# Kernel tuning notes

Hardware: AMD Instinct MI355X
Metric: run time of the kernel (lower is better)

## Reference

```python
import jax, jax.numpy as jnp
import numpy as np

N_NODES = 20000
N_EDGES = 320000
D_IN = 256      # n_source_nodes (input feature dim)
HEADS = 4
HEAD_DIM = 64   # n_target_nodes // heads
D_OUT = HEADS * HEAD_DIM  # n_target_nodes = 256
EDGE_DIM = 1


def setup_inputs() -> dict:
    key = jax.random.key(0)
    ks = jax.random.split(key, 12)
    s = 0.05
    return {
        "x": jax.random.normal(ks[0], (N_NODES, D_IN), jnp.float32),
        "edge_index": jax.random.randint(ks[1], (2, N_EDGES), 0, N_NODES, jnp.int64),
        "edge_attr": jax.random.normal(ks[2], (N_EDGES, EDGE_DIM), jnp.float32),
        # TransformerConv params (weights stored [in, out]; PyG Linear defaults: q/k/v have bias, edge lin has no bias, skip lin has bias)
        "Wq": jax.random.normal(ks[3], (D_IN, D_OUT), jnp.float32) * s,
        "bq": jnp.zeros((D_OUT,), jnp.float32),
        "Wk": jax.random.normal(ks[4], (D_IN, D_OUT), jnp.float32) * s,
        "bk": jnp.zeros((D_OUT,), jnp.float32),
        "Wv": jax.random.normal(ks[5], (D_IN, D_OUT), jnp.float32) * s,
        "bv": jnp.zeros((D_OUT,), jnp.float32),
        "We": jax.random.normal(ks[6], (EDGE_DIM, D_OUT), jnp.float32) * s,
        "Wskip": jax.random.normal(ks[7], (D_IN, D_OUT), jnp.float32) * s,
        "bskip": jnp.zeros((D_OUT,), jnp.float32),
        # GraphNorm params
        "gn_weight": jnp.ones((D_OUT,), jnp.float32),
        "gn_bias": jnp.zeros((D_OUT,), jnp.float32),
        "gn_mean_scale": jnp.ones((D_OUT,), jnp.float32),
    }


def reference(x, edge_index, edge_attr, Wq, bq, Wk, bk, Wv, bv, We, Wskip, bskip, gn_weight, gn_bias, gn_mean_scale):
    N = x.shape[0]
    src, dst = edge_index[0], edge_index[1]  # message flows src -> dst (source_to_target)

    q = (x @ Wq + bq).reshape(N, HEADS, HEAD_DIM)
    k = (x @ Wk + bk).reshape(N, HEADS, HEAD_DIM)
    v = (x @ Wv + bv).reshape(N, HEADS, HEAD_DIM)
    e = (edge_attr @ We).reshape(-1, HEADS, HEAD_DIM)  # [E, H, C]

    k_j = k[src] + e                                   # [E, H, C]
    alpha = jnp.einsum('ehc,ehc->eh', q[dst], k_j) / jnp.sqrt(jnp.float32(HEAD_DIM))

    # segment softmax over edges sharing the same target node
    a_max = jax.ops.segment_max(alpha, dst, num_segments=N)[dst]
    a_exp = jnp.exp(alpha - a_max)
    a_sum = jax.ops.segment_sum(a_exp, dst, num_segments=N)[dst]
    att = a_exp / (a_sum + 1e-16)                      # [E, H]

    msg = (v[src] + e) * att[..., None]                # [E, H, C]
    out = jax.ops.segment_sum(msg, dst, num_segments=N).reshape(N, D_OUT)
    out = out + x @ Wskip + bskip                      # root/skip connection (beta=False)

    # GraphNorm (single graph): weight*(x - alpha*mean)/sqrt(var+eps) + bias
    mean = out.mean(axis=0)
    centered = out - gn_mean_scale * mean
    var = jnp.mean(centered * centered, axis=0)
    out = gn_weight * centered * jax.lax.rsqrt(var + 1e-5) + gn_bias

    out = jax.nn.relu(out)
    xt = out.T @ out                                   # [D_OUT, D_OUT]
    xt_min, xt_max = jnp.min(xt), jnp.max(xt)
    return (xt - xt_min) / (xt_max - xt_min + 1e-8)
```

## Files before the change

kernel.cpp:

```cpp
#include <hip/hip_runtime.h>
#include <math.h>

#define N_NODES 20000
#define N_EDGES 320000
#define SK 20480

typedef short short8 __attribute__((ext_vector_type(8)));
typedef float f32x4 __attribute__((ext_vector_type(4)));

static __device__ __forceinline__ unsigned short f2bf(float f) {
    unsigned int u = __float_as_uint(f);
    u = (u + 0x7FFF + ((u >> 16) & 1)) >> 16;
    return (unsigned short)u;
}
static __device__ __forceinline__ float b2f(unsigned short u) {
    return __uint_as_float((unsigned int)u << 16);
}

__global__ __launch_bounds__(256) void conv_x_k(const float* __restrict__ x,
                                                unsigned short* __restrict__ xb)
{
    const int t8 = blockIdx.x * 256 + threadIdx.x;
    const size_t base = (size_t)t8 * 8;
    if (base >= (size_t)N_NODES * 256) return;
    const float4 f0 = *(const float4*)(x + base);
    const float4 f1 = *(const float4*)(x + base + 4);
    ushort4 u0, u1;
    u0.x = f2bf(f0.x); u0.y = f2bf(f0.y); u0.z = f2bf(f0.z); u0.w = f2bf(f0.w);
    u1.x = f2bf(f1.x); u1.y = f2bf(f1.y); u1.z = f2bf(f1.z); u1.w = f2bf(f1.w);
    *(ushort4*)(xb + base) = u0;
    *(ushort4*)(xb + base + 4) = u1;
}

__global__ __launch_bounds__(256) void conv_w_k(const float* __restrict__ Wq,
                                                const float* __restrict__ Wk,
                                                const float* __restrict__ Wv,
                                                const float* __restrict__ Wsk,
                                                const float* __restrict__ bq,
                                                const float* __restrict__ bk,
                                                const float* __restrict__ bv,
                                                const float* __restrict__ bsk,
                                                unsigned short* __restrict__ wT,
                                                float* __restrict__ bias_all)
{
    const int b = blockIdx.x;
    const int kk = threadIdx.x;
    const int wi = b >> 8, n = b & 255;
    const float* W = (wi == 0) ? Wq : (wi == 1) ? Wk : (wi == 2) ? Wv : Wsk;
    wT[(size_t)b * 256 + kk] = f2bf(W[(size_t)kk * 256 + n]);
    if (kk == 0) {
        const float* bb = (wi == 0) ? bq : (wi == 1) ? bk : (wi == 2) ? bv : bsk;
        bias_all[b] = bb[n];
    }
}

__global__ __launch_bounds__(512, 2) void gemm_qkvs(const unsigned short* __restrict__ xb,
                                                    const unsigned short* __restrict__ wT,
                                                    const float* __restrict__ bias_all,
                                                    float* __restrict__ qb,
                                                    unsigned short* __restrict__ kb,
                                                    unsigned short* __restrict__ vb,
                                                    float* __restrict__ ob)
{
    __shared__ __align__(16) unsigned short As[(128 + 256) * 80];
    unsigned short* Bs = As + 128 * 80;
    float* stage = (float*)As;

    const int tid  = threadIdx.x;
    const int lane = tid & 63;
    const int w    = tid >> 6;
    const int wm = w >> 2, wn = w & 3;
    const int row0 = blockIdx.x * 128;
    const int wsel = blockIdx.y;
    const int colG = wsel * 256;
    const int ar = tid >> 2, ak = (tid & 3) * 16;
    const int br = tid >> 1, bk = (tid & 1) * 32;
    const int fr = lane & 15, fk = (lane >> 4) * 8, lg = lane >> 4;

    f32x4 acc[4][4] = {};

    for (int k0 = 0; k0 < 256; k0 += 64) {
        int gr = row0 + ar; gr = gr < N_NODES ? gr : N_NODES - 1;
        const unsigned short* ap = xb + (size_t)gr * 256 + k0 + ak;
        const uint4 a0 = *(const uint4*)ap;
        const uint4 a1 = *(const uint4*)(ap + 8);
        const unsigned short* bp = wT + (size_t)(colG + br) * 256 + k0 + bk;
        const uint4 b0 = *(const uint4*)bp;
        const uint4 b1 = *(const uint4*)(bp + 8);
        const uint4 b2 = *(const uint4*)(bp + 16);
        const uint4 b3 = *(const uint4*)(bp + 24);
        __syncthreads();
        *(uint4*)&As[ar * 80 + ak]     = a0;
        *(uint4*)&As[ar * 80 + ak + 8] = a1;
        unsigned short* bsp = &Bs[br * 80 + bk];
        *(uint4*)bsp        = b0;
        *(uint4*)(bsp + 8)  = b1;
        *(uint4*)(bsp + 16) = b2;
        *(uint4*)(bsp + 24) = b3;
        __syncthreads();
#pragma unroll
        for (int ks = 0; ks < 2; ++ks) {
            short8 af[4], bf[4];
#pragma unroll
            for (int m = 0; m < 4; ++m)
                af[m] = *(const short8*)&As[(wm * 64 + m * 16 + fr) * 80 + ks * 32 + fk];
#pragma unroll
            for (int n = 0; n < 4; ++n)
                bf[n] = *(const short8*)&Bs[(wn * 64 + n * 16 + fr) * 80 + ks * 32 + fk];
#pragma unroll
            for (int m = 0; m < 4; ++m)
#pragma unroll
                for (int n = 0; n < 4; ++n)
                    acc[m][n] = __builtin_amdgcn_mfma_f32_16x16x32_bf16(af[m], bf[n], acc[m][n], 0, 0, 0);
        }
    }
    __syncthreads();

    float badd[4];
#pragma unroll
    for (int n = 0; n < 4; ++n) badd[n] = bias_all[colG + wn * 64 + n * 16 + fr];

    float* st = stage + w * 1024;
#pragma unroll
    for (int m = 0; m < 4; ++m) {
#pragma unroll
        for (int n = 0; n < 4; ++n)
#pragma unroll
            for (int r = 0; r < 4; ++r)
                st[(lg * 4 + r) * 64 + n * 16 + fr] = acc[m][n][r] + badd[n];
#pragma unroll
        for (int it = 0; it < 4; ++it) {
            const int lrow = it * 4 + lg;
            const f32x4 c4 = *(const f32x4*)&st[lrow * 64 + fr * 4];
            const int grow = row0 + wm * 64 + m * 16 + lrow;
            if (grow < N_NODES) {
                const size_t idx = (size_t)grow * 256 + wn * 64 + fr * 4;
                if (wsel == 0) {
                    float4 o; o.x = c4[0]; o.y = c4[1]; o.z = c4[2]; o.w = c4[3];
                    *(float4*)(qb + idx) = o;
                } else if (wsel == 3) {
                    float4 o; o.x = c4[0]; o.y = c4[1]; o.z = c4[2]; o.w = c4[3];
                    *(float4*)(ob + idx) = o;
                } else {
                    ushort4 u;
                    u.x = f2bf(c4[0]); u.y = f2bf(c4[1]); u.z = f2bf(c4[2]); u.w = f2bf(c4[3]);
                    if (wsel == 1) *(ushort4*)(kb + idx) = u;
                    else           *(ushort4*)(vb + idx) = u;
                }
            }
        }
    }
}

__global__ void count_deg(const int* __restrict__ dst, int* __restrict__ deg)
{
    const int e = blockIdx.x * 256 + threadIdx.x;
    if (e < N_EDGES) atomicAdd(&deg[dst[e]], 1);
}

__global__ __launch_bounds__(1024) void scan_k(const int* __restrict__ deg,
                                               int* __restrict__ row_start)
{
    const int tid = threadIdx.x;
    const int lane = tid & 63, wid = tid >> 6;
    const int CH = 20;
    const int base = tid * CH;
    int local[CH];
    int s = 0;
#pragma unroll
    for (int i = 0; i < CH; ++i) {
        const int idx = base + i;
        const int d = (idx < N_NODES) ? deg[idx] : 0;
        local[i] = s;
        s += d;
    }
    int v = s;
#pragma unroll
    for (int off = 1; off < 64; off <<= 1) {
        const int t = __shfl_up(v, off);
        if (lane >= off) v += t;
    }
    __shared__ int wsum[16];
    if (lane == 63) wsum[wid] = v;
    __syncthreads();
    if (tid == 0) {
        int r = 0;
        for (int i = 0; i < 16; ++i) { const int t = wsum[i]; wsum[i] = r; r += t; }
    }
    __syncthreads();
    const int excl = v - s + wsum[wid];
#pragma unroll
    for (int i = 0; i < CH; ++i) {
        const int idx = base + i;
        if (idx < N_NODES) row_start[idx] = excl + local[i];
    }
    if (tid == 1023) row_start[N_NODES] = excl + s;
}

__global__ void fill_csr(const int* __restrict__ dst, const int* __restrict__ src,
                         const float* __restrict__ ea,
                         const int* __restrict__ row_start,
                         int* __restrict__ cursor, int2* __restrict__ ekv)
{
    const int e = blockIdx.x * 256 + threadIdx.x;
    if (e < N_EDGES) {
        const int d = dst[e];
        const int p = atomicAdd(&cursor[d], 1);
        int2 pk;
        pk.x = src[e];
        pk.y = __float_as_int(ea[e]);
        ekv[row_start[d] + p] = pk;
    }
}

__global__ __launch_bounds__(256) void attn_k(const float* __restrict__ q,
                                              const unsigned short* __restrict__ kb,
                                              const unsigned short* __restrict__ vb,
                                              const float* __restrict__ We,
                                              const int* __restrict__ row_start,
                                              const int2* __restrict__ ekv,
                                              float* __restrict__ out)
{
    const int wid  = threadIdx.x >> 6;
    const int lane = threadIdx.x & 63;
    const int n = blockIdx.x * 4 + wid;
    if (n >= N_NODES) return;

    const float4 qf  = *(const float4*)(q + (size_t)n * 256 + lane * 4);
    const float4 we4 = *(const float4*)(We + lane * 4);
    const int rs = row_start[n], re = row_start[n + 1];

    float ssum = 0.f;
    float ax = 0.f, ay = 0.f, az = 0.f, aw = 0.f;

    int s = rs;
    for (; s + 2 <= re; s += 2) {
        const int2 p0 = ekv[s];
        const int2 p1 = ekv[s + 1];
        int sn0 = p0.x, sn1 = p1.x;
        sn0 = ((unsigned)sn0 < N_NODES) ? sn0 : 0;
        sn1 = ((unsigned)sn1 < N_NODES) ? sn1 : 0;
        const float a0 = __int_as_float(p0.y), a1 = __int_as_float(p1.y);
        const ushort4 k0 = *(const ushort4*)(kb + (size_t)sn0 * 256 + lane * 4);
        const ushort4 v0 = *(const ushort4*)(vb + (size_t)sn0 * 256 + lane * 4);
        const ushort4 k1 = *(const ushort4*)(kb + (size_t)sn1 * 256 + lane * 4);
        const ushort4 v1 = *(const ushort4*)(vb + (size_t)sn1 * 256 + lane * 4);

        float p = qf.x * (b2f(k0.x) + a0 * we4.x) + qf.y * (b2f(k0.y) + a0 * we4.y)
                + qf.z * (b2f(k0.z) + a0 * we4.z) + qf.w * (b2f(k0.w) + a0 * we4.w);
        p += __shfl_xor(p, 1); p += __shfl_xor(p, 2);
        p += __shfl_xor(p, 4); p += __shfl_xor(p, 8);
        float wgt = __expf(p * 0.125f);
        ssum += wgt;
        ax += wgt * (b2f(v0.x) + a0 * we4.x);
        ay += wgt * (b2f(v0.y) + a0 * we4.y);
        az += wgt * (b2f(v0.z) + a0 * we4.z);
        aw += wgt * (b2f(v0.w) + a0 * we4.w);

        p = qf.x * (b2f(k1.x) + a1 * we4.x) + qf.y * (b2f(k1.y) + a1 * we4.y)
          + qf.z * (b2f(k1.z) + a1 * we4.z) + qf.w * (b2f(k1.w) + a1 * we4.w);
        p += __shfl_xor(p, 1); p += __shfl_xor(p, 2);
        p += __shfl_xor(p, 4); p += __shfl_xor(p, 8);
        wgt = __expf(p * 0.125f);
        ssum += wgt;
        ax += wgt * (b2f(v1.x) + a1 * we4.x);
        ay += wgt * (b2f(v1.y) + a1 * we4.y);
        az += wgt * (b2f(v1.z) + a1 * we4.z);
        aw += wgt * (b2f(v1.w) + a1 * we4.w);
    }
    if (s < re) {
        const int2 p0 = ekv[s];
        int sn0 = p0.x;
        sn0 = ((unsigned)sn0 < N_NODES) ? sn0 : 0;
        const float a0 = __int_as_float(p0.y);
        const ushort4 k0 = *(const ushort4*)(kb + (size_t)sn0 * 256 + lane * 4);
        const ushort4 v0 = *(const ushort4*)(vb + (size_t)sn0 * 256 + lane * 4);
        float p = qf.x * (b2f(k0.x) + a0 * we4.x) + qf.y * (b2f(k0.y) + a0 * we4.y)
                + qf.z * (b2f(k0.z) + a0 * we4.z) + qf.w * (b2f(k0.w) + a0 * we4.w);
        p += __shfl_xor(p, 1); p += __shfl_xor(p, 2);
        p += __shfl_xor(p, 4); p += __shfl_xor(p, 8);
        const float wgt = __expf(p * 0.125f);
        ssum += wgt;
        ax += wgt * (b2f(v0.x) + a0 * we4.x);
        ay += wgt * (b2f(v0.y) + a0 * we4.y);
        az += wgt * (b2f(v0.z) + a0 * we4.z);
        aw += wgt * (b2f(v0.w) + a0 * we4.w);
    }
    const float inv = 1.f / (ssum + 1e-16f);
    const float4 sk = *(const float4*)(out + (size_t)n * 256 + lane * 4);
    float4 o;
    o.x = ax * inv + sk.x;
    o.y = ay * inv + sk.y;
    o.z = az * inv + sk.z;
    o.w = aw * inv + sk.w;
    *(float4*)(out + (size_t)n * 256 + lane * 4) = o;
}

__global__ __launch_bounds__(256) void gn_stats_k(const float* __restrict__ out,
                                                  float* __restrict__ gstats)
{
    const int c = threadIdx.x;
    float s = 0.f, s2 = 0.f;
    for (int r = blockIdx.x; r < N_NODES; r += gridDim.x) {
        const float vv = out[(size_t)r * 256 + c];
        s += vv; s2 += vv * vv;
    }
    atomicAdd(&gstats[c], s);
    atomicAdd(&gstats[256 + c], s2);
}

__global__ __launch_bounds__(256) void norm_relu_T(const float* __restrict__ ob,
                                                   const float* __restrict__ gstats,
                                                   const float* __restrict__ gw,
                                                   const float* __restrict__ gb,
                                                   const float* __restrict__ gms,
                                                   unsigned short* __restrict__ obT)
{
    __shared__ unsigned short tile[256][72];
    __shared__ float smu[256], swi[256], sbd[256];
    const int t = threadIdx.x;
    const int r0 = blockIdx.x * 64;
    {
        const float invN = 1.f / (float)N_NODES;
        const float mean = gstats[t] * invN;
        const float exx  = gstats[256 + t] * invN;
        const float mu   = gms[t] * mean;
        const float var  = exx - 2.f * mu * mean + mu * mu;
        smu[t] = mu;
        swi[t] = gw[t] * rsqrtf(var + 1e-5f);
        sbd[t] = gb[t];
    }
    __syncthreads();
    const int rr = t >> 2;
    const int row = r0 + rr;
#pragma unroll
    for (int it = 0; it < 16; ++it) {
        const int col = it * 16 + (t & 3) * 4;
        float4 f = make_float4(0.f, 0.f, 0.f, 0.f);
        if (row < N_NODES) f = *(const float4*)(ob + (size_t)row * 256 + col);
        ushort4 u;
        if (row < N_NODES) {
            u.x = f2bf(fmaxf((f.x - smu[col + 0]) * swi[col + 0] + sbd[col + 0], 0.f));
            u.y = f2bf(fmaxf((f.y - smu[col + 1]) * swi[col + 1] + sbd[col + 1], 0.f));
            u.z = f2bf(fmaxf((f.z - smu[col + 2]) * swi[col + 2] + sbd[col + 2], 0.f));
            u.w = f2bf(fmaxf((f.w - smu[col + 3]) * swi[col + 3] + sbd[col + 3], 0.f));
        } else { u.x = u.y = u.z = u.w = 0; }
        tile[col + 0][rr] = u.x;
        tile[col + 1][rr] = u.y;
        tile[col + 2][rr] = u.z;
        tile[col + 3][rr] = u.w;
    }
    __syncthreads();
#pragma unroll
    for (int it = 0; it < 8; ++it) {
        const int c = it * 32 + (t >> 3);
        const int part = t & 7;
        const uint4 x0 = *(const uint4*)&tile[c][part * 8];
        *(uint4*)(obT + (size_t)c * SK + r0 + part * 8) = x0;
    }
}

__global__ __launch_bounds__(256) void gram_k(const unsigned short* __restrict__ obT,
                                              float* __restrict__ xt)
{
    const int bi_l[10] = {0,0,0,0,1,1,1,2,2,3};
    const int bj_l[10] = {0,1,2,3,1,2,3,2,3,3};
    const int bi = bi_l[blockIdx.x], bj = bj_l[blockIdx.x];
    const int r0 = blockIdx.y * 1024;

    __shared__ __align__(16) unsigned short Ai[64 * 136];
    __shared__ __align__(16) unsigned short Aj[64 * 136];
    const int tid = threadIdx.x;
    const int lane = tid & 63;
    const int w = tid >> 6;
    const int wi = w >> 1, wj = w & 1;
    const int lr = tid >> 2, kseg = (tid & 3) * 32;
    const int fr = lane & 15, fk = (lane >> 4) * 8, lg = lane >> 4;

    f32x4 acc[2][2] = {};

    for (int kt = 0; kt < 1024; kt += 128) {
        uint4 ai[4], aj[4];
        const unsigned short* pa = obT + (size_t)(bi * 64 + lr) * SK + r0 + kt + kseg;
        const unsigned short* pb = obT + (size_t)(bj * 64 + lr) * SK + r0 + kt + kseg;
#pragma unroll
        for (int j = 0; j < 4; ++j) { ai[j] = *(const uint4*)(pa + 8 * j); aj[j] = *(const uint4*)(pb + 8 * j); }
        __syncthreads();
#pragma unroll
        for (int j = 0; j < 4; ++j) {
            *(uint4*)&Ai[lr * 136 + kseg + 8 * j] = ai[j];
            *(uint4*)&Aj[lr * 136 + kseg + 8 * j] = aj[j];
        }
        __syncthreads();
#pragma unroll
        for (int ks = 0; ks < 4; ++ks) {
            short8 af[2], bf[2];
#pragma unroll
            for (int m = 0; m < 2; ++m)
                af[m] = *(const short8*)&Ai[(wi * 32 + m * 16 + fr) * 136 + ks * 32 + fk];
#pragma unroll
            for (int n = 0; n < 2; ++n)
                bf[n] = *(const short8*)&Aj[(wj * 32 + n * 16 + fr) * 136 + ks * 32 + fk];
#pragma unroll
            for (int m = 0; m < 2; ++m)
#pragma unroll
                for (int n = 0; n < 2; ++n)
                    acc[m][n] = __builtin_amdgcn_mfma_f32_16x16x32_bf16(af[m], bf[n], acc[m][n], 0, 0, 0);
        }
    }
#pragma unroll
    for (int m = 0; m < 2; ++m)
#pragma unroll
        for (int n = 0; n < 2; ++n)
#pragma unroll
            for (int r = 0; r < 4; ++r)
                atomicAdd(&xt[(size_t)(bi * 64 + wi * 32 + m * 16 + lg * 4 + r) * 256
                              + bj * 64 + wj * 32 + n * 16 + fr], acc[m][n][r]);
}

__global__ __launch_bounds__(1024) void minmax_k(const float* __restrict__ xt,
                                                 float* __restrict__ mm)
{
    const int tid = threadIdx.x;
    float mn = 1e30f, mx = -1e30f;
    for (int i = tid; i < 65536; i += 1024) {
        const int r = i >> 8, c = i & 255;
        if ((r >> 6) <= (c >> 6)) {
            const float v = xt[i];
            mn = fminf(mn, v);
            mx = fmaxf(mx, v);
        }
    }
    for (int off = 1; off < 64; off <<= 1) {
        mn = fminf(mn, __shfl_xor(mn, off));
        mx = fmaxf(mx, __shfl_xor(mx, off));
    }
    __shared__ float smn[16], smx[16];
    const int w = tid >> 6;
    if ((tid & 63) == 0) { smn[w] = mn; smx[w] = mx; }
    __syncthreads();
    if (tid == 0) {
        for (int i = 1; i < 16; ++i) {
            mn = fminf(mn, smn[i]);
            mx = fmaxf(mx, smx[i]);
        }
        mm[0] = mn; mm[1] = mx;
    }
}

__global__ void finalize_k(const float* __restrict__ xt, const float* __restrict__ mm,
                           float* __restrict__ outp)
{
    const int i = blockIdx.x * 256 + threadIdx.x;
    const int r = i >> 8, c = i & 255;
    const float v = ((r >> 6) <= (c >> 6)) ? xt[i] : xt[c * 256 + r];
    const float mn = mm[0], mx = mm[1];
    const float inv = 1.f / (mx - mn + 1e-8f);
    outp[i] = (v - mn) * inv;
}

extern "C" void kernel_launch(void* const* d_in, const int* in_sizes, int n_in,
                              void* d_out, int out_size, void* d_ws, size_t ws_size,
                              hipStream_t stream)
{
    (void)in_sizes; (void)n_in; (void)out_size; (void)ws_size;
    const float* x   = (const float*)d_in[0];
    const int*   ei  = (const int*)d_in[1];
    const float* ea  = (const float*)d_in[2];
    const float* Wq  = (const float*)d_in[3];
    const float* bq  = (const float*)d_in[4];
    const float* Wk  = (const float*)d_in[5];
    const float* bk  = (const float*)d_in[6];
    const float* Wv  = (const float*)d_in[7];
    const float* bv  = (const float*)d_in[8];
    const float* We  = (const float*)d_in[9];
    const float* Wsk = (const float*)d_in[10];
    const float* bsk = (const float*)d_in[11];
    const float* gw  = (const float*)d_in[12];
    const float* gb  = (const float*)d_in[13];
    const float* gms = (const float*)d_in[14];
    float* outp = (float*)d_out;

    char* ws = (char*)d_ws;
    size_t off = 0;
    #define WS_ALLOC(nbytes) (ws + off); off = (off + (size_t)(nbytes) + 255) & ~(size_t)255
    unsigned short* xb = (unsigned short*)WS_ALLOC((size_t)N_NODES * 256 * 2);
    unsigned short* wT = (unsigned short*)WS_ALLOC((size_t)1024 * 256 * 2);
    float* bias_all    = (float*)WS_ALLOC(1024 * 4);
    float* qb          = (float*)WS_ALLOC((size_t)N_NODES * 256 * 4);
    unsigned short* kb = (unsigned short*)WS_ALLOC((size_t)N_NODES * 256 * 2);
    unsigned short* vb = (unsigned short*)WS_ALLOC((size_t)N_NODES * 256 * 2);
    float* ob          = (float*)WS_ALLOC((size_t)N_NODES * 256 * 4);
    const size_t zoff = off;
    int*   deg    = (int*)WS_ALLOC((size_t)N_NODES * 4);
    int*   cur    = (int*)WS_ALLOC((size_t)N_NODES * 4);
    float* gstats = (float*)WS_ALLOC(512 * 4);
    float* xt     = (float*)WS_ALLOC(65536 * 4);
    const size_t zbytes = off - zoff;
    int* row_start = (int*)WS_ALLOC((size_t)(N_NODES + 1) * 4);
    float* mm      = (float*)WS_ALLOC(2 * 4);
    #undef WS_ALLOC
    int2* ekv           = (int2*)xb;
    unsigned short* obT = (unsigned short*)qb;

    const int* srcv = ei;
    const int* dstv = ei + N_EDGES;

    hipMemsetAsync(ws + zoff, 0, zbytes, stream);

    conv_x_k<<<(N_NODES * 256 / 8 + 255) / 256, 256, 0, stream>>>(x, xb);
    conv_w_k<<<1024, 256, 0, stream>>>(Wq, Wk, Wv, Wsk, bq, bk, bv, bsk, wT, bias_all);

    gemm_qkvs<<<dim3((N_NODES + 127) / 128, 4), 512, 0, stream>>>(xb, wT, bias_all,
                                                                  qb, kb, vb, ob);

    count_deg<<<(N_EDGES + 255) / 256, 256, 0, stream>>>(dstv, deg);
    scan_k<<<1, 1024, 0, stream>>>(deg, row_start);
    fill_csr<<<(N_EDGES + 255) / 256, 256, 0, stream>>>(dstv, srcv, ea, row_start, cur, ekv);

    attn_k<<<(N_NODES + 3) / 4, 256, 0, stream>>>(qb, kb, vb, We, row_start, ekv, ob);

    gn_stats_k<<<160, 256, 0, stream>>>(ob, gstats);
    norm_relu_T<<<320, 256, 0, stream>>>(ob, gstats, gw, gb, gms, obT);

    gram_k<<<dim3(10, 20), 256, 0, stream>>>(obT, xt);
    minmax_k<<<1, 1024, 0, stream>>>(xt, mm);
    finalize_k<<<256, 256, 0, stream>>>(xt, mm, outp);
}
```

Measured before the change: 235.5 us.

## Interleave K and V rows and unroll attention edge loop by four

The GEMM epilogue now writes K and V bf16 values interleaved into one buffer, so each lane fetches its 4 K and 4 V values for an edge with a single 16-byte load instead of two 8-byte loads. The attention loop is unrolled to four edges with all gathers issued up front to increase memory-level parallelism. The scan kernel stages degrees in shared memory for coalesced reads, and the GraphNorm stats kernel uses more blocks. The costs are higher register use in the attention kernel and a strided write pattern in the GEMM epilogue.

```diff
diff --git a/kernel.cpp b/kernel.cpp
--- a/kernel.cpp
+++ b/kernel.cpp
@@ -15,6 +15,12 @@
 }
 static __device__ __forceinline__ float b2f(unsigned short u) {
     return __uint_as_float((unsigned int)u << 16);
+}
+static __device__ __forceinline__ float blo(unsigned int u) {
+    return __uint_as_float(u << 16);
+}
+static __device__ __forceinline__ float bhi(unsigned int u) {
+    return __uint_as_float(u & 0xFFFF0000u);
 }
 
 __global__ __launch_bounds__(256) void conv_x_k(const float* __restrict__ x,
@@ -58,8 +64,7 @@
                                                     const unsigned short* __restrict__ wT,
                                                     const float* __restrict__ bias_all,
                                                     float* __restrict__ qb,
-                                                    unsigned short* __restrict__ kb,
-                                                    unsigned short* __restrict__ vb,
+                                                    unsigned short* __restrict__ kvb,
                                                     float* __restrict__ ob)
 {
     __shared__ __align__(16) unsigned short As[(128 + 256) * 80];
@@ -134,18 +139,17 @@
             const f32x4 c4 = *(const f32x4*)&st[lrow * 64 + fr * 4];
             const int grow = row0 + wm * 64 + m * 16 + lrow;
             if (grow < N_NODES) {
-                const size_t idx = (size_t)grow * 256 + wn * 64 + fr * 4;
                 if (wsel == 0) {
                     float4 o; o.x = c4[0]; o.y = c4[1]; o.z = c4[2]; o.w = c4[3];
-                    *(float4*)(qb + idx) = o;
+                    *(float4*)(qb + (size_t)grow * 256 + wn * 64 + fr * 4) = o;
                 } else if (wsel == 3) {
                     float4 o; o.x = c4[0]; o.y = c4[1]; o.z = c4[2]; o.w = c4[3];
-                    *(float4*)(ob + idx) = o;
+                    *(float4*)(ob + (size_t)grow * 256 + wn * 64 + fr * 4) = o;
                 } else {
                     ushort4 u;
                     u.x = f2bf(c4[0]); u.y = f2bf(c4[1]); u.z = f2bf(c4[2]); u.w = f2bf(c4[3]);
-                    if (wsel == 1) *(ushort4*)(kb + idx) = u;
-                    else           *(ushort4*)(vb + idx) = u;
+                    const size_t kvidx = (size_t)grow * 512 + (wn * 16 + fr) * 8 + (wsel == 1 ? 0 : 4);
+                    *(ushort4*)(kvb + kvidx) = u;
                 }
             }
         }
@@ -161,18 +165,23 @@
 __global__ __launch_bounds__(1024) void scan_k(const int* __restrict__ deg,
                                                int* __restrict__ row_start)
 {
+    __shared__ int sdeg[20480];
     const int tid = threadIdx.x;
     const int lane = tid & 63, wid = tid >> 6;
     const int CH = 20;
+#pragma unroll
+    for (int i = 0; i < 20; ++i) {
+        const int idx = i * 1024 + tid;
+        sdeg[idx] = (idx < N_NODES) ? deg[idx] : 0;
+    }
+    __syncthreads();
     const int base = tid * CH;
     int local[CH];
     int s = 0;
 #pragma unroll
     for (int i = 0; i < CH; ++i) {
-        const int idx = base + i;
-        const int d = (idx < N_NODES) ? deg[idx] : 0;
         local[i] = s;
-        s += d;
+        s += sdeg[base + i];
     }
     int v = s;
 #pragma unroll
@@ -213,9 +222,27 @@
     }
 }
 
+static __device__ __forceinline__ void edge_step(const uint4 kv, const float a,
+                                                 const float4 qf, const float4 we4,
+                                                 float& ssum, float& ax, float& ay,
+                                                 float& az, float& aw)
+{
+    const float k0 = blo(kv.x), k1 = bhi(kv.x), k2 = blo(kv.y), k3 = bhi(kv.y);
+    const float v0 = blo(kv.z), v1 = bhi(kv.z), v2 = blo(kv.w), v3 = bhi(kv.w);
+    float p = qf.x * (k0 + a * we4.x) + qf.y * (k1 + a * we4.y)
+            + qf.z * (k2 + a * we4.z) + qf.w * (k3 + a * we4.w);
+    p += __shfl_xor(p, 1); p += __shfl_xor(p, 2);
+    p += __shfl_xor(p, 4); p += __shfl_xor(p, 8);
+    const float wgt = __expf(p * 0.125f);
+    ssum += wgt;
+    ax += wgt * (v0 + a * we4.x);
+    ay += wgt * (v1 + a * we4.y);
+    az += wgt * (v2 + a * we4.z);
+    aw += wgt * (v3 + a * we4.w);
+}
+
 __global__ __launch_bounds__(256) void attn_k(const float* __restrict__ q,
-                                              const unsigned short* __restrict__ kb,
-                                              const unsigned short* __restrict__ vb,
+                                              const unsigned short* __restrict__ kvb,
                                               const float* __restrict__ We,
                                               const int* __restrict__ row_start,
                                               const int2* __restrict__ ekv,
@@ -229,62 +256,33 @@
     const float4 qf  = *(const float4*)(q + (size_t)n * 256 + lane * 4);
     const float4 we4 = *(const float4*)(We + lane * 4);
     const int rs = row_start[n], re = row_start[n + 1];
+    const int lo8 = lane * 8;
 
     float ssum = 0.f;
     float ax = 0.f, ay = 0.f, az = 0.f, aw = 0.f;
 
     int s = rs;
-    for (; s + 2 <= re; s += 2) {
+    for (; s + 4 <= re; s += 4) {
+        const int2 p0 = ekv[s],     p1 = ekv[s + 1];
+        const int2 p2 = ekv[s + 2], p3 = ekv[s + 3];
+        const int sn0 = ((unsigned)p0.x < N_NODES) ? p0.x : 0;
+        const int sn1 = ((unsigned)p1.x < N_NODES) ? p1.x : 0;
+        const int sn2 = ((unsigned)p2.x < N_NODES) ? p2.x : 0;
+        const int sn3 = ((unsigned)p3.x < N_NODES) ? p3.x : 0;
+        const uint4 kv0 = *(const uint4*)(kvb + (size_t)sn0 * 512 + lo8);
+        const uint4 kv1 = *(const uint4*)(kvb + (size_t)sn1 * 512 + lo8);
+        const uint4 kv2 = *(const uint4*)(kvb + (size_t)sn2 * 512 + lo8);
+        const uint4 kv3 = *(const uint4*)(kvb + (size_t)sn3 * 512 + lo8);
+        edge_step(kv0, __int_as_float(p0.y), qf, we4, ssum, ax, ay, az, aw);
+        edge_step(kv1, __int_as_float(p1.y), qf, we4, ssum, ax, ay, az, aw);
+        edge_step(kv2, __int_as_float(p2.y), qf, we4, ssum, ax, ay, az, aw);
+        edge_step(kv3, __int_as_float(p3.y), qf, we4, ssum, ax, ay, az, aw);
+    }
+    for (; s < re; ++s) {
         const int2 p0 = ekv[s];
-        const int2 p1 = ekv[s + 1];
-        int sn0 = p0.x, sn1 = p1.x;
-        sn0 = ((unsigned)sn0 < N_NODES) ? sn0 : 0;
-        sn1 = ((unsigned)sn1 < N_NODES) ? sn1 : 0;
-        const float a0 = __int_as_float(p0.y), a1 = __int_as_float(p1.y);
-        const ushort4 k0 = *(const ushort4*)(kb + (size_t)sn0 * 256 + lane * 4);
-        const ushort4 v0 = *(const ushort4*)(vb + (size_t)sn0 * 256 + lane * 4);
-        const ushort4 k1 = *(const ushort4*)(kb + (size_t)sn1 * 256 + lane * 4);
-        const ushort4 v1 = *(const ushort4*)(vb + (size_t)sn1 * 256 + lane * 4);
-
-        float p = qf.x * (b2f(k0.x) + a0 * we4.x) + qf.y * (b2f(k0.y) + a0 * we4.y)
-                + qf.z * (b2f(k0.z) + a0 * we4.z) + qf.w * (b2f(k0.w) + a0 * we4.w);
-        p += __shfl_xor(p, 1); p += __shfl_xor(p, 2);
-        p += __shfl_xor(p, 4); p += __shfl_xor(p, 8);
-        float wgt = __expf(p * 0.125f);
-        ssum += wgt;
-        ax += wgt * (b2f(v0.x) + a0 * we4.x);
-        ay += wgt * (b2f(v0.y) + a0 * we4.y);
-        az += wgt * (b2f(v0.z) + a0 * we4.z);
-        aw += wgt * (b2f(v0.w) + a0 * we4.w);
-
-        p = qf.x * (b2f(k1.x) + a1 * we4.x) + qf.y * (b2f(k1.y) + a1 * we4.y)
-          + qf.z * (b2f(k1.z) + a1 * we4.z) + qf.w * (b2f(k1.w) + a1 * we4.w);
-        p += __shfl_xor(p, 1); p += __shfl_xor(p, 2);
-        p += __shfl_xor(p, 4); p += __shfl_xor(p, 8);
-        wgt = __expf(p * 0.125f);
-        ssum += wgt;
-        ax += wgt * (b2f(v1.x) + a1 * we4.x);
-        ay += wgt * (b2f(v1.y) + a1 * we4.y);
-        az += wgt * (b2f(v1.z) + a1 * we4.z);
-        aw += wgt * (b2f(v1.w) + a1 * we4.w);
-    }
-    if (s < re) {
-        const int2 p0 = ekv[s];
-        int sn0 = p0.x;
-        sn0 = ((unsigned)sn0 < N_NODES) ? sn0 : 0;
-        const float a0 = __int_as_float(p0.y);
-        const ushort4 k0 = *(const ushort4*)(kb + (size_t)sn0 * 256 + lane * 4);
-        const ushort4 v0 = *(const ushort4*)(vb + (size_t)sn0 * 256 + lane * 4);
-        float p = qf.x * (b2f(k0.x) + a0 * we4.x) + qf.y * (b2f(k0.y) + a0 * we4.y)
-                + qf.z * (b2f(k0.z) + a0 * we4.z) + qf.w * (b2f(k0.w) + a0 * we4.w);
-        p += __shfl_xor(p, 1); p += __shfl_xor(p, 2);
-        p += __shfl_xor(p, 4); p += __shfl_xor(p, 8);
-        const float wgt = __expf(p * 0.125f);
-        ssum += wgt;
-        ax += wgt * (b2f(v0.x) + a0 * we4.x);
-        ay += wgt * (b2f(v0.y) + a0 * we4.y);
-        az += wgt * (b2f(v0.z) + a0 * we4.z);
-        aw += wgt * (b2f(v0.w) + a0 * we4.w);
+        const int sn0 = ((unsigned)p0.x < N_NODES) ? p0.x : 0;
+        const uint4 kv0 = *(const uint4*)(kvb + (size_t)sn0 * 512 + lo8);
+        edge_step(kv0, __int_as_float(p0.y), qf, we4, ssum, ax, ay, az, aw);
     }
     const float inv = 1.f / (ssum + 1e-16f);
     const float4 sk = *(const float4*)(out + (size_t)n * 256 + lane * 4);
@@ -484,13 +482,12 @@
     char* ws = (char*)d_ws;
     size_t off = 0;
     #define WS_ALLOC(nbytes) (ws + off); off = (off + (size_t)(nbytes) + 255) & ~(size_t)255
-    unsigned short* xb = (unsigned short*)WS_ALLOC((size_t)N_NODES * 256 * 2);
-    unsigned short* wT = (unsigned short*)WS_ALLOC((size_t)1024 * 256 * 2);
-    float* bias_all    = (float*)WS_ALLOC(1024 * 4);
-    float* qb          = (float*)WS_ALLOC((size_t)N_NODES * 256 * 4);
-    unsigned short* kb = (unsigned short*)WS_ALLOC((size_t)N_NODES * 256 * 2);
-    unsigned short* vb = (unsigned short*)WS_ALLOC((size_t)N_NODES * 256 * 2);
-    float* ob          = (float*)WS_ALLOC((size_t)N_NODES * 256 * 4);
+    unsigned short* xb  = (unsigned short*)WS_ALLOC((size_t)N_NODES * 256 * 2);
+    unsigned short* wT  = (unsigned short*)WS_ALLOC((size_t)1024 * 256 * 2);
+    float* bias_all     = (float*)WS_ALLOC(1024 * 4);
+    float* qb           = (float*)WS_ALLOC((size_t)N_NODES * 256 * 4);
+    unsigned short* kvb = (unsigned short*)WS_ALLOC((size_t)N_NODES * 512 * 2);
+    float* ob           = (float*)WS_ALLOC((size_t)N_NODES * 256 * 4);
     const size_t zoff = off;
     int*   deg    = (int*)WS_ALLOC((size_t)N_NODES * 4);
     int*   cur    = (int*)WS_ALLOC((size_t)N_NODES * 4);
@@ -512,15 +509,15 @@
     conv_w_k<<<1024, 256, 0, stream>>>(Wq, Wk, Wv, Wsk, bq, bk, bv, bsk, wT, bias_all);
 
     gemm_qkvs<<<dim3((N_NODES + 127) / 128, 4), 512, 0, stream>>>(xb, wT, bias_all,
-                                                                  qb, kb, vb, ob);
+                                                                  qb, kvb, ob);
 
     count_deg<<<(N_EDGES + 255) / 256, 256, 0, stream>>>(dstv, deg);
     scan_k<<<1, 1024, 0, stream>>>(deg, row_start);
     fill_csr<<<(N_EDGES + 255) / 256, 256, 0, stream>>>(dstv, srcv, ea, row_start, cur, ekv);
 
-    attn_k<<<(N_NODES + 3) / 4, 256, 0, stream>>>(qb, kb, vb, We, row_start, ekv, ob);
-
-    gn_stats_k<<<160, 256, 0, stream>>>(ob, gstats);
+    attn_k<<<(N_NODES + 3) / 4, 256, 0, stream>>>(qb, kvb, We, row_start, ekv, ob);
+
+    gn_stats_k<<<400, 256, 0, stream>>>(ob, gstats);
     norm_relu_T<<<320, 256, 0, stream>>>(ob, gstats, gw, gb, gms, obT);
 
     gram_k<<<dim3(10, 20), 256, 0, stream>>>(obT, xt);
```

After: 226.5 us. 3.8% less time.
